# Optimization experiments

Measured on AMD Instinct MI355X. Metric: run time of the kernel, lower is better.

Reference implementation:

```python
import jax, jax.numpy as jnp
import numpy as np

DIM_A, DIM_V, DIM_D = 256, 256, 256
B, N = 16, 1024

def _levi_civita():
    e = np.zeros((3, 3, 3), dtype=np.float32)
    e[0, 1, 2] = e[1, 2, 0] = e[2, 0, 1] = 1.0
    e[0, 2, 1] = e[2, 1, 0] = e[1, 0, 2] = -1.0
    return jnp.asarray(e)

EPS = _levi_civita()
EYE3 = jnp.eye(3, dtype=jnp.float32)

def setup_inputs() -> dict:
    key = jax.random.key(0)
    ks = jax.random.split(key, 8)
    def w(k, dout, din):
        return jax.random.normal(k, (dout, din), dtype=jnp.float32) * (din ** -0.5)
    return {
        "x_a": jax.random.normal(ks[0], (B, N, DIM_A), dtype=jnp.float32),
        "x_v": jax.random.normal(ks[1], (B, N, DIM_V, 3), dtype=jnp.float32),
        "x_d": jax.random.normal(ks[2], (B, N, DIM_D, 3, 3), dtype=jnp.float32),
        "W_ttrans": w(ks[3], DIM_D, DIM_D),   # TensTrans(2,0,1,dim_d,dim_d).lin.W
        "W_ttrace": w(ks[4], DIM_A, DIM_D),   # TensTrace(2,dim_d,dim_a).lin.W
        "W_tdelta": w(ks[5], DIM_D, DIM_A),   # TensDelta(0,dim_a,dim_d).lin.W
        "W_vd": w(ks[6], DIM_D, DIM_V),       # ChiralMix.lin_vd.W
        "W_dv": w(ks[7], DIM_V, DIM_D),       # ChiralMix.lin_dv.W
    }

def reference(x_a, x_v, x_d, W_ttrans, W_ttrace, W_tdelta, W_vd, W_dv):
    # TensTrans: swap the two spatial indices, then channel linear
    x_d = x_d + jnp.einsum('oc,bncji->bnoij', W_ttrans, x_d)
    # TensTrace: trace over spatial dims, then channel linear -> scalar channel
    x_a_new = x_a + jnp.einsum('oc,bncii->bno', W_ttrace, x_d)
    # TensDelta: channel linear on scalars, expand with delta_ij
    x_d = x_d + jnp.einsum('oc,bnc->bno', W_tdelta, x_a)[..., None, None] * EYE3
    x_a = x_a_new
    # ChiralMix: eps-contract d->v then linear; linear v->d then eps-expand
    dv = jnp.einsum('oc,bncij,ijk->bnok', W_dv, x_d, EPS)       # [B,N,dim_v,3]
    vd = jnp.einsum('oc,bnci,ijk->bnokj', W_vd, x_v, EPS)       # [B,N,dim_d,3,3]
    return (x_a, x_v + dv, x_d + vd)
```

## Files before the change

kernel.cpp:

```cpp
#include <hip/hip_runtime.h>

typedef __attribute__((ext_vector_type(8))) short bf16x8;
typedef __attribute__((ext_vector_type(4))) float f32x4;

#define TM 8

__device__ __forceinline__ unsigned short f2bf(float f) {
    unsigned u = __builtin_bit_cast(unsigned, f);
    u += 0x7FFFu + ((u >> 16) & 1u);
    return (unsigned short)(u >> 16);
}
__device__ __forceinline__ float bf2f(unsigned short h) {
    return __builtin_bit_cast(float, (unsigned)h << 16);
}

__device__ __forceinline__ int widx(int w, int o, int c) {
    int tile = o >> 4, col = o & 15;
    int ks = c >> 5, aq = (c >> 3) & 3, j = c & 7;
    return (((tile * 8 + ks) * 6 + w) * 64 + aq * 16 + col) * 8 + j;
}

__global__ __launch_bounds__(512)
void avd_prep_kernel(const float* __restrict__ Wtt, const float* __restrict__ Wtr,
                     const float* __restrict__ Wtd, const float* __restrict__ Wvd,
                     const float* __restrict__ Wdv, unsigned short* __restrict__ ws)
{
    __shared__ float ra[2][256], rv[2][256];
    const int half = threadIdx.x >> 8;
    const int c    = threadIdx.x & 255;
    const int o    = blockIdx.x * 2 + half;
    ra[half][c] = Wtr[o * 256 + c];
    rv[half][c] = Wdv[o * 256 + c];
    __syncthreads();
    float sa = 0.f, sv = 0.f;
    #pragma unroll 8
    for (int k = 0; k < 256; ++k) {
        float w = Wtt[k * 256 + c];
        sa += ra[half][k] * w;
        sv += rv[half][k] * w;
    }
    const int idx = o * 256 + c;
    const float wa = Wtr[idx] + sa;
    const float wv = Wdv[idx] - sv;
    ws[widx(0, o, c)] = f2bf(Wtt[idx]);
    ws[widx(1, o, c)] = f2bf(Wtd[idx]);
    ws[widx(2, o, c)] = f2bf(Wvd[idx]);
    ws[widx(3, o, c)] = f2bf(wa);
    ws[widx(4, o, c)] = f2bf(wv);
    ws[widx(5, o, c)] = f2bf(-wv);
}

__global__ __launch_bounds__(512, 4)
void avd_main_kernel(const float* __restrict__ xa, const float* __restrict__ xv,
                     const float* __restrict__ xd,
                     const unsigned short* __restrict__ ws,
                     float* __restrict__ out)
{
    __shared__ __attribute__((aligned(16))) unsigned short feat[104][264];

    const int tid  = threadIdx.x;
    const int lane = tid & 63;
    const int wid  = tid >> 6;
    const int m0   = blockIdx.x * TM;

    float* out_xa = out;
    float* out_xv = out + 4194304;
    float* out_xd = out + 16777216;

    {
        const int m  = wid;
        const int mx = m << 3;
        const f32x4* srcd = (const f32x4*)(xd + (size_t)(m0 + m) * 2304);
        #pragma unroll
        for (int it = 0; it < 9; ++it) {
            int ch = lane + it * 64;
            f32x4 v = __builtin_nontemporal_load(&srcd[ch]);
            int e0 = ch * 4;
            #pragma unroll
            for (int j = 0; j < 4; ++j) {
                int e = e0 + j;
                int c = e / 9;
                int q = e - c * 9;
                feat[m * 13 + q][c ^ mx] = f2bf(v[j]);
            }
        }
        const f32x4* srcv = (const f32x4*)(xv + (size_t)(m0 + m) * 768);
        #pragma unroll
        for (int it = 0; it < 3; ++it) {
            int ch = lane + it * 64;
            f32x4 v = __builtin_nontemporal_load(&srcv[ch]);
            int e0 = ch * 4;
            #pragma unroll
            for (int j = 0; j < 4; ++j) {
                int e = e0 + j;
                int c = e / 3;
                int i = e - c * 3;
                feat[m * 13 + 10 + i][c ^ mx] = f2bf(v[j]);
            }
        }
        {
            f32x4 v = __builtin_nontemporal_load(&((const f32x4*)(xa + (size_t)(m0 + m) * 256))[lane]);
            #pragma unroll
            for (int j = 0; j < 4; ++j)
                feat[m * 13 + 9][(lane * 4 + j) ^ mx] = f2bf(v[j]);
        }
    }
    __syncthreads();

    const int am  = lane & 7;
    const int aq  = lane >> 4;
    const int col = lane & 15;

    #pragma unroll 1
    for (int t = 0; t < 2; ++t) {
        const int o = t * 128 + wid * 16 + col;

        f32x4 acc[17];
        #pragma unroll
        for (int p = 0; p < 17; ++p) acc[p] = (f32x4){0.f, 0.f, 0.f, 0.f};

        #pragma unroll 2
        for (int ks = 0; ks < 8; ++ks) {
            const int csw = (ks * 32 + aq * 8) ^ (am << 3);
            bf16x8 a[13];
            #pragma unroll
            for (int p = 0; p < 13; ++p)
                a[p] = *(const bf16x8*)&feat[am * 13 + p][csw];

            const unsigned short* wsb = ws + ((((t * 8 + wid) * 8 + ks) * 6) * 64 + lane) * 8;
            bf16x8 b_tt = *(const bf16x8*)(wsb + 0 * 512);
            bf16x8 b_td = *(const bf16x8*)(wsb + 1 * 512);
            bf16x8 b_vd = *(const bf16x8*)(wsb + 2 * 512);
            bf16x8 b_wa = *(const bf16x8*)(wsb + 3 * 512);
            bf16x8 b_wv = *(const bf16x8*)(wsb + 4 * 512);
            bf16x8 b_wn = *(const bf16x8*)(wsb + 5 * 512);

            #pragma unroll
            for (int q = 0; q < 9; ++q)
                acc[q] = __builtin_amdgcn_mfma_f32_16x16x32_bf16(a[q], b_tt, acc[q], 0, 0, 0);
            acc[9]  = __builtin_amdgcn_mfma_f32_16x16x32_bf16(a[9],  b_td, acc[9],  0, 0, 0);
            acc[10] = __builtin_amdgcn_mfma_f32_16x16x32_bf16(a[10], b_vd, acc[10], 0, 0, 0);
            acc[11] = __builtin_amdgcn_mfma_f32_16x16x32_bf16(a[11], b_vd, acc[11], 0, 0, 0);
            acc[12] = __builtin_amdgcn_mfma_f32_16x16x32_bf16(a[12], b_vd, acc[12], 0, 0, 0);
            acc[13] = __builtin_amdgcn_mfma_f32_16x16x32_bf16(a[0], b_wa, acc[13], 0, 0, 0);
            acc[13] = __builtin_amdgcn_mfma_f32_16x16x32_bf16(a[4], b_wa, acc[13], 0, 0, 0);
            acc[13] = __builtin_amdgcn_mfma_f32_16x16x32_bf16(a[8], b_wa, acc[13], 0, 0, 0);
            acc[14] = __builtin_amdgcn_mfma_f32_16x16x32_bf16(a[5], b_wv, acc[14], 0, 0, 0);
            acc[14] = __builtin_amdgcn_mfma_f32_16x16x32_bf16(a[7], b_wn, acc[14], 0, 0, 0);
            acc[15] = __builtin_amdgcn_mfma_f32_16x16x32_bf16(a[6], b_wv, acc[15], 0, 0, 0);
            acc[15] = __builtin_amdgcn_mfma_f32_16x16x32_bf16(a[2], b_wn, acc[15], 0, 0, 0);
            acc[16] = __builtin_amdgcn_mfma_f32_16x16x32_bf16(a[1], b_wv, acc[16], 0, 0, 0);
            acc[16] = __builtin_amdgcn_mfma_f32_16x16x32_bf16(a[3], b_wn, acc[16], 0, 0, 0);
        }

        {
            const int hi = (lane >> 4) & 1;
#define EPI(R)                                                                  \
            {                                                                   \
                const int m   = hi * 4 + (R);                                   \
                const int cso = o ^ (m << 3);                                   \
                float d[9];                                                     \
                _Pragma("unroll")                                               \
                for (int q = 0; q < 9; ++q) d[q] = bf2f(feat[m * 13 + q][cso]); \
                const float delta = acc[9][(R)];                                \
                const float w0 = acc[10][(R)], w1 = acc[11][(R)], w2 = acc[12][(R)]; \
                const size_t row = (size_t)(m0 + m) * 256 + o;                  \
                float* po = out_xd + row * 9;                                   \
                po[0] = d[0] + acc[0][(R)] + delta;                             \
                po[1] = d[1] + acc[3][(R)] - w2;                                \
                po[2] = d[2] + acc[6][(R)] + w1;                                \
                po[3] = d[3] + acc[1][(R)] + w2;                                \
                po[4] = d[4] + acc[4][(R)] + delta;                             \
                po[5] = d[5] + acc[7][(R)] - w0;                                \
                po[6] = d[6] + acc[2][(R)] - w1;                                \
                po[7] = d[7] + acc[5][(R)] + w0;                                \
                po[8] = d[8] + acc[8][(R)] + delta;                             \
                out_xa[row] = bf2f(feat[m * 13 + 9][cso]) + acc[13][(R)];       \
                const size_t vrow = row * 3;                                    \
                out_xv[vrow + 0] = bf2f(feat[m * 13 + 10][cso]) + acc[14][(R)]; \
                out_xv[vrow + 1] = bf2f(feat[m * 13 + 11][cso]) + acc[15][(R)]; \
                out_xv[vrow + 2] = bf2f(feat[m * 13 + 12][cso]) + acc[16][(R)]; \
            }
            if (lane < 32) { EPI(0); EPI(1); }
            else           { EPI(2); EPI(3); }
#undef EPI
        }
    }
}

extern "C" void kernel_launch(void* const* d_in, const int* in_sizes, int n_in,
                              void* d_out, int out_size, void* d_ws, size_t ws_size,
                              hipStream_t stream) {
    const float* xa  = (const float*)d_in[0];
    const float* xv  = (const float*)d_in[1];
    const float* xd  = (const float*)d_in[2];
    const float* Wtt = (const float*)d_in[3];
    const float* Wtr = (const float*)d_in[4];
    const float* Wtd = (const float*)d_in[5];
    const float* Wvd = (const float*)d_in[6];
    const float* Wdv = (const float*)d_in[7];
    unsigned short* ws = (unsigned short*)d_ws;
    float* out = (float*)d_out;

    avd_prep_kernel<<<dim3(128), dim3(512), 0, stream>>>(Wtt, Wtr, Wtd, Wvd, Wdv, ws);
    avd_main_kernel<<<dim3(16384 / TM), dim3(512), 0, stream>>>(xa, xv, xd, ws, out);
}
```

Measured before the change: 166.0 us.

## Pack paired feature rows into MFMA tiles and split results with permlane32 swap

With TM=8, each 16-row MFMA A-tile holds only 8 real rows. This change fills the spare rows with a second feature component, so one MFMA computes two components. It cuts the MFMA count per k-step from 21 to 13. Afterwards v_permlane32_swap separates the packed halves, and the negated dv weight block is dropped in favour of a subtraction in the epilogue. The cost is some cross-lane permute work, plus reliance on the accumulator row layout splitting the two halves across lanes 0-31 and 32-63.

```diff
diff --git a/kernel.cpp b/kernel.cpp
--- a/kernel.cpp
+++ b/kernel.cpp
@@ -17,7 +17,7 @@
 __device__ __forceinline__ int widx(int w, int o, int c) {
     int tile = o >> 4, col = o & 15;
     int ks = c >> 5, aq = (c >> 3) & 3, j = c & 7;
-    return (((tile * 8 + ks) * 6 + w) * 64 + aq * 16 + col) * 8 + j;
+    return (((tile * 8 + ks) * 5 + w) * 64 + aq * 16 + col) * 8 + j;
 }
 
 __global__ __launch_bounds__(512)
@@ -40,14 +40,11 @@
         sv += rv[half][k] * w;
     }
     const int idx = o * 256 + c;
-    const float wa = Wtr[idx] + sa;
-    const float wv = Wdv[idx] - sv;
     ws[widx(0, o, c)] = f2bf(Wtt[idx]);
     ws[widx(1, o, c)] = f2bf(Wtd[idx]);
     ws[widx(2, o, c)] = f2bf(Wvd[idx]);
-    ws[widx(3, o, c)] = f2bf(wa);
-    ws[widx(4, o, c)] = f2bf(wv);
-    ws[widx(5, o, c)] = f2bf(-wv);
+    ws[widx(3, o, c)] = f2bf(Wtr[idx] + sa);
+    ws[widx(4, o, c)] = f2bf(Wdv[idx] - sv);
 }
 
 __global__ __launch_bounds__(512, 4)
@@ -115,43 +112,59 @@
     for (int t = 0; t < 2; ++t) {
         const int o = t * 128 + wid * 16 + col;
 
-        f32x4 acc[17];
-        #pragma unroll
-        for (int p = 0; p < 17; ++p) acc[p] = (f32x4){0.f, 0.f, 0.f, 0.f};
+        f32x4 cP0{}, cP1{}, cP2{}, cP3{};
+        f32x4 cS8{}, cSd{};
+        f32x4 cW01{}, cW2{};
+        f32x4 cA04{}, cA8{};
+        f32x4 cV57{}, cV62{}, cV13{};
 
         #pragma unroll 2
         for (int ks = 0; ks < 8; ++ks) {
             const int csw = (ks * 32 + aq * 8) ^ (am << 3);
-            bf16x8 a[13];
-            #pragma unroll
-            for (int p = 0; p < 13; ++p)
-                a[p] = *(const bf16x8*)&feat[am * 13 + p][csw];
-
-            const unsigned short* wsb = ws + ((((t * 8 + wid) * 8 + ks) * 6) * 64 + lane) * 8;
+            const unsigned short* fb = &feat[am * 13][csw];
+#define AP(qa, qb) (*(const bf16x8*)(fb + ((lane & 8) ? (qb) : (qa)) * 264))
+#define AD(q)      (*(const bf16x8*)(fb + (q) * 264))
+            bf16x8 a01 = AP(0, 1),  a23 = AP(2, 3), a45 = AP(4, 5), a67 = AP(6, 7);
+            bf16x8 a8  = AD(8),     a9  = AD(9);
+            bf16x8 aW  = AP(10, 11), aW2 = AD(12);
+            bf16x8 a04 = AP(0, 4),  a57 = AP(5, 7), a62 = AP(6, 2), a13 = AP(1, 3);
+#undef AP
+#undef AD
+            const unsigned short* wsb = ws + ((((t * 8 + wid) * 8 + ks) * 5) * 64 + lane) * 8;
             bf16x8 b_tt = *(const bf16x8*)(wsb + 0 * 512);
             bf16x8 b_td = *(const bf16x8*)(wsb + 1 * 512);
             bf16x8 b_vd = *(const bf16x8*)(wsb + 2 * 512);
             bf16x8 b_wa = *(const bf16x8*)(wsb + 3 * 512);
             bf16x8 b_wv = *(const bf16x8*)(wsb + 4 * 512);
-            bf16x8 b_wn = *(const bf16x8*)(wsb + 5 * 512);
-
-            #pragma unroll
-            for (int q = 0; q < 9; ++q)
-                acc[q] = __builtin_amdgcn_mfma_f32_16x16x32_bf16(a[q], b_tt, acc[q], 0, 0, 0);
-            acc[9]  = __builtin_amdgcn_mfma_f32_16x16x32_bf16(a[9],  b_td, acc[9],  0, 0, 0);
-            acc[10] = __builtin_amdgcn_mfma_f32_16x16x32_bf16(a[10], b_vd, acc[10], 0, 0, 0);
-            acc[11] = __builtin_amdgcn_mfma_f32_16x16x32_bf16(a[11], b_vd, acc[11], 0, 0, 0);
-            acc[12] = __builtin_amdgcn_mfma_f32_16x16x32_bf16(a[12], b_vd, acc[12], 0, 0, 0);
-            acc[13] = __builtin_amdgcn_mfma_f32_16x16x32_bf16(a[0], b_wa, acc[13], 0, 0, 0);
-            acc[13] = __builtin_amdgcn_mfma_f32_16x16x32_bf16(a[4], b_wa, acc[13], 0, 0, 0);
-            acc[13] = __builtin_amdgcn_mfma_f32_16x16x32_bf16(a[8], b_wa, acc[13], 0, 0, 0);
-            acc[14] = __builtin_amdgcn_mfma_f32_16x16x32_bf16(a[5], b_wv, acc[14], 0, 0, 0);
-            acc[14] = __builtin_amdgcn_mfma_f32_16x16x32_bf16(a[7], b_wn, acc[14], 0, 0, 0);
-            acc[15] = __builtin_amdgcn_mfma_f32_16x16x32_bf16(a[6], b_wv, acc[15], 0, 0, 0);
-            acc[15] = __builtin_amdgcn_mfma_f32_16x16x32_bf16(a[2], b_wn, acc[15], 0, 0, 0);
-            acc[16] = __builtin_amdgcn_mfma_f32_16x16x32_bf16(a[1], b_wv, acc[16], 0, 0, 0);
-            acc[16] = __builtin_amdgcn_mfma_f32_16x16x32_bf16(a[3], b_wn, acc[16], 0, 0, 0);
-        }
+
+            cP0  = __builtin_amdgcn_mfma_f32_16x16x32_bf16(a01, b_tt, cP0, 0, 0, 0);
+            cP1  = __builtin_amdgcn_mfma_f32_16x16x32_bf16(a23, b_tt, cP1, 0, 0, 0);
+            cP2  = __builtin_amdgcn_mfma_f32_16x16x32_bf16(a45, b_tt, cP2, 0, 0, 0);
+            cP3  = __builtin_amdgcn_mfma_f32_16x16x32_bf16(a67, b_tt, cP3, 0, 0, 0);
+            cS8  = __builtin_amdgcn_mfma_f32_16x16x32_bf16(a8,  b_tt, cS8, 0, 0, 0);
+            cSd  = __builtin_amdgcn_mfma_f32_16x16x32_bf16(a9,  b_td, cSd, 0, 0, 0);
+            cW01 = __builtin_amdgcn_mfma_f32_16x16x32_bf16(aW,  b_vd, cW01, 0, 0, 0);
+            cW2  = __builtin_amdgcn_mfma_f32_16x16x32_bf16(aW2, b_vd, cW2, 0, 0, 0);
+            cA04 = __builtin_amdgcn_mfma_f32_16x16x32_bf16(a04, b_wa, cA04, 0, 0, 0);
+            cA8  = __builtin_amdgcn_mfma_f32_16x16x32_bf16(a8,  b_wa, cA8, 0, 0, 0);
+            cV57 = __builtin_amdgcn_mfma_f32_16x16x32_bf16(a57, b_wv, cV57, 0, 0, 0);
+            cV62 = __builtin_amdgcn_mfma_f32_16x16x32_bf16(a62, b_wv, cV62, 0, 0, 0);
+            cV13 = __builtin_amdgcn_mfma_f32_16x16x32_bf16(a13, b_wv, cV13, 0, 0, 0);
+        }
+
+#define SWAPEO(e, oo, src) { \
+            _Pragma("unroll") \
+            for (int j = 0; j < 4; ++j) { \
+                float a_ = (src)[j], b_ = (src)[j]; \
+                asm volatile("v_permlane32_swap_b32 %0, %1" : "+v"(a_), "+v"(b_)); \
+                (e)[j] = a_; (oo)[j] = b_; } }
+        f32x4 t0v, t1v, t2v, t3v, t4v, t5v, t6v, t7v;
+        f32x4 w0v, w1v, xa0v, xa4v, a5v, a7v, a6v, a2v, a1v, a3v;
+        SWAPEO(t0v, t1v, cP0);  SWAPEO(t2v, t3v, cP1);
+        SWAPEO(t4v, t5v, cP2);  SWAPEO(t6v, t7v, cP3);
+        SWAPEO(w0v, w1v, cW01); SWAPEO(xa0v, xa4v, cA04);
+        SWAPEO(a5v, a7v, cV57); SWAPEO(a6v, a2v, cV62); SWAPEO(a1v, a3v, cV13);
+#undef SWAPEO
 
         {
             const int hi = (lane >> 4) & 1;
@@ -162,24 +175,24 @@
                 float d[9];                                                     \
                 _Pragma("unroll")                                               \
                 for (int q = 0; q < 9; ++q) d[q] = bf2f(feat[m * 13 + q][cso]); \
-                const float delta = acc[9][(R)];                                \
-                const float w0 = acc[10][(R)], w1 = acc[11][(R)], w2 = acc[12][(R)]; \
+                const float delta = cSd[(R)];                                   \
+                const float w0 = w0v[(R)], w1 = w1v[(R)], w2 = cW2[(R)];        \
                 const size_t row = (size_t)(m0 + m) * 256 + o;                  \
                 float* po = out_xd + row * 9;                                   \
-                po[0] = d[0] + acc[0][(R)] + delta;                             \
-                po[1] = d[1] + acc[3][(R)] - w2;                                \
-                po[2] = d[2] + acc[6][(R)] + w1;                                \
-                po[3] = d[3] + acc[1][(R)] + w2;                                \
-                po[4] = d[4] + acc[4][(R)] + delta;                             \
-                po[5] = d[5] + acc[7][(R)] - w0;                                \
-                po[6] = d[6] + acc[2][(R)] - w1;                                \
-                po[7] = d[7] + acc[5][(R)] + w0;                                \
-                po[8] = d[8] + acc[8][(R)] + delta;                             \
-                out_xa[row] = bf2f(feat[m * 13 + 9][cso]) + acc[13][(R)];       \
+                po[0] = d[0] + t0v[(R)] + delta;                                \
+                po[1] = d[1] + t3v[(R)] - w2;                                   \
+                po[2] = d[2] + t6v[(R)] + w1;                                   \
+                po[3] = d[3] + t1v[(R)] + w2;                                   \
+                po[4] = d[4] + t4v[(R)] + delta;                                \
+                po[5] = d[5] + t7v[(R)] - w0;                                   \
+                po[6] = d[6] + t2v[(R)] - w1;                                   \
+                po[7] = d[7] + t5v[(R)] + w0;                                   \
+                po[8] = d[8] + cS8[(R)] + delta;                                \
+                out_xa[row] = bf2f(feat[m * 13 + 9][cso]) + xa0v[(R)] + xa4v[(R)] + cA8[(R)]; \
                 const size_t vrow = row * 3;                                    \
-                out_xv[vrow + 0] = bf2f(feat[m * 13 + 10][cso]) + acc[14][(R)]; \
-                out_xv[vrow + 1] = bf2f(feat[m * 13 + 11][cso]) + acc[15][(R)]; \
-                out_xv[vrow + 2] = bf2f(feat[m * 13 + 12][cso]) + acc[16][(R)]; \
+                out_xv[vrow + 0] = bf2f(feat[m * 13 + 10][cso]) + a5v[(R)] - a7v[(R)]; \
+                out_xv[vrow + 1] = bf2f(feat[m * 13 + 11][cso]) + a6v[(R)] - a2v[(R)]; \
+                out_xv[vrow + 2] = bf2f(feat[m * 13 + 12][cso]) + a1v[(R)] - a3v[(R)]; \
             }
             if (lane < 32) { EPI(0); EPI(1); }
             else           { EPI(2); EPI(3); }
```

Result: faster. 144.3 us (-13.1%).
